# Kernel optimization log

Hardware: AMD Instinct MI355X
Metric: run time of the kernel (lower is better)

Reference implementation:

```python
import jax, jax.numpy as jnp
import numpy as np

NEG_SLOPE = 0.2
EPS = 1e-16

def gatv2(x, edge_index, edge_attr, Wl, bl, We, att, bias):
    """PyG GATv2Conv, heads=1, share_weights=True, with edge_dim."""
    N = x.shape[0]
    h = x @ Wl + bl                      # [N, out] shared lin_l == lin_r
    src, dst = edge_index[0], edge_index[1]
    hj = h[src]                          # source (message) features [E, out]
    hi = h[dst]                          # target features [E, out]
    e = jax.nn.leaky_relu(hi + hj + edge_attr @ We, NEG_SLOPE)  # [E, out]
    score = e @ att                      # [E]
    # segment softmax over edges grouped by destination node
    smax = jax.ops.segment_max(score, dst, num_segments=N)
    ex = jnp.exp(score - smax[dst])
    denom = jax.ops.segment_sum(ex, dst, num_segments=N)
    alpha = ex / (denom[dst] + EPS)      # [E]
    out = jax.ops.segment_sum(hj * alpha[:, None], dst, num_segments=N)
    return out + bias


def setup_inputs() -> dict:
    key = jax.random.key(0)
    N, E = 50000, 800000
    D_IN, D_LAT, D_EDGE, N_ACT = 128, 128, 16, 32
    ks = jax.random.split(key, 16)
    s = 0.05
    inp = {
        "x": jax.random.normal(ks[0], (N, D_IN), jnp.float32),
        "edge_index": jax.random.randint(ks[1], (2, E), 0, N, jnp.int32),
        "edge_attr": jax.random.normal(ks[2], (E, D_EDGE), jnp.float32),
        # gnn_layer: D_IN -> D_LAT
        "Wl1": jax.random.normal(ks[3], (D_IN, D_LAT), jnp.float32) * s,
        "bl1": jnp.zeros((D_LAT,), jnp.float32),
        "We1": jax.random.normal(ks[4], (D_EDGE, D_LAT), jnp.float32) * s,
        "att1": jax.random.normal(ks[5], (D_LAT,), jnp.float32) * s,
        "bias1": jnp.zeros((D_LAT,), jnp.float32),
        # node_layer: D_LAT -> 1
        "Wl2": jax.random.normal(ks[6], (D_LAT, 1), jnp.float32) * s,
        "bl2": jnp.zeros((1,), jnp.float32),
        "We2": jax.random.normal(ks[7], (D_EDGE, 1), jnp.float32) * s,
        "att2": jax.random.normal(ks[8], (1,), jnp.float32) * s,
        "bias2": jnp.zeros((1,), jnp.float32),
        # action_layer: D_LAT -> N_ACT
        "Wl3": jax.random.normal(ks[9], (D_LAT, N_ACT), jnp.float32) * s,
        "bl3": jnp.zeros((N_ACT,), jnp.float32),
        "We3": jax.random.normal(ks[10], (D_EDGE, N_ACT), jnp.float32) * s,
        "att3": jax.random.normal(ks[11], (N_ACT,), jnp.float32) * s,
        "bias3": jnp.zeros((N_ACT,), jnp.float32),
    }
    return inp


def reference(x, edge_index, edge_attr,
              Wl1, bl1, We1, att1, bias1,
              Wl2, bl2, We2, att2, bias2,
              Wl3, bl3, We3, att3, bias3):
    latent = gatv2(x, edge_index, edge_attr, Wl1, bl1, We1, att1, bias1)          # [N, D_LAT]
    node_logits = gatv2(latent, edge_index, edge_attr, Wl2, bl2, We2, att2, bias2)[:, 0]  # [N]
    action_logits = gatv2(latent, edge_index, edge_attr, Wl3, bl3, We3, att3, bias3)      # [N, A]
    # categorical sampling with fixed key (deterministic reference)
    k1, k2 = jax.random.split(jax.random.key(42))
    node_sel = jax.random.categorical(k1, node_logits)
    node_lp = jax.nn.log_softmax(node_logits)[node_sel]
    act_logits_sel = action_logits[node_sel, :]
    action_sel = jax.random.categorical(k2, act_logits_sel)
    action_lp = jax.nn.log_softmax(act_logits_sel)[action_sel]
    return (node_sel, action_sel, node_lp + action_lp)
```

## Files before the change

### kernel.cpp

```cpp
#include <hip/hip_runtime.h>
#include <stdint.h>
#include <math.h>

#define NEG 0.2f
#define TINYF 1.1754943508222875e-38f

typedef float f4 __attribute__((ext_vector_type(4)));
typedef float f2 __attribute__((ext_vector_type(2)));

__host__ __device__ inline void threefry2x32(uint32_t k0, uint32_t k1,
                                             uint32_t x0, uint32_t x1,
                                             uint32_t* o0, uint32_t* o1) {
  uint32_t ks0 = k0, ks1 = k1, ks2 = k0 ^ k1 ^ 0x1BD11BDAu;
  x0 += ks0; x1 += ks1;
#define RR(r) { x0 += x1; x1 = (x1 << (r)) | (x1 >> (32 - (r))); x1 ^= x0; }
  RR(13) RR(15) RR(26) RR(6)
  x0 += ks1; x1 += ks2 + 1u;
  RR(17) RR(29) RR(16) RR(24)
  x0 += ks2; x1 += ks0 + 2u;
  RR(13) RR(15) RR(26) RR(6)
  x0 += ks0; x1 += ks1 + 3u;
  RR(17) RR(29) RR(16) RR(24)
  x0 += ks1; x1 += ks2 + 4u;
  RR(13) RR(15) RR(26) RR(6)
  x0 += ks2; x1 += ks0 + 5u;
#undef RR
  *o0 = x0; *o1 = x1;
}

__device__ inline float gumbel_part(uint32_t ka, uint32_t kb, uint32_t i) {
  uint32_t o0, o1;
  threefry2x32(ka, kb, 0u, i, &o0, &o1);
  uint32_t bits = o0 ^ o1;
  float f = __uint_as_float((bits >> 9) | 0x3f800000u) - 1.0f;
  float u = fmaxf(TINYF, f + TINYF);
  return -logf(-logf(u));
}

__global__ void count_kernel(const int* __restrict__ ei, int E, int* __restrict__ counts) {
  int e = blockIdx.x * blockDim.x + threadIdx.x;
  if (e < E) atomicAdd(&counts[ei[E + e]], 1);
}

#define SCB 256
__global__ __launch_bounds__(256) void scan_partial_kernel(const int* __restrict__ counts,
    int N, int chunk, int* __restrict__ bsum) {
  int b = blockIdx.x;
  int s0 = b * chunk, s1 = s0 + chunk; if (s1 > N) s1 = N;
  int tid = threadIdx.x;
  int v = 0;
  for (int i = s0 + tid; i < s1; i += 256) v += counts[i];
  __shared__ int red[256];
  red[tid] = v; __syncthreads();
  for (int s = 128; s; s >>= 1) { if (tid < s) red[tid] += red[tid + s]; __syncthreads(); }
  if (tid == 0) bsum[b] = red[0];
}

__global__ __launch_bounds__(256) void scan_offsets_kernel(const int* __restrict__ bsum,
    int* __restrict__ boff, int* __restrict__ row_start, int N) {
  int tid = threadIdx.x; int lane = tid & 63; int wv = tid >> 6;
  __shared__ int wsum[4];
  int v = bsum[tid];
  int incl = v;
#pragma unroll
  for (int off = 1; off < 64; off <<= 1) {
    int t = __shfl_up(incl, off);
    if (lane >= off) incl += t;
  }
  if (lane == 63) wsum[wv] = incl;
  __syncthreads();
  if (tid == 0) {
    int s = 0;
    for (int k = 0; k < 4; k++) { int t = wsum[k]; wsum[k] = s; s += t; }
    row_start[N] = s;
  }
  __syncthreads();
  boff[tid] = wsum[wv] + incl - v;
}

__global__ __launch_bounds__(256) void scan_apply_kernel(const int* __restrict__ counts,
    const int* __restrict__ boff, int N, int chunk,
    int* __restrict__ row_start, int* __restrict__ cursor) {
  int b = blockIdx.x;
  int s0 = b * chunk, s1 = s0 + chunk; if (s1 > N) s1 = N;
  int tid = threadIdx.x; int lane = tid & 63; int wv = tid >> 6;
  __shared__ int wsum[4];
  __shared__ int tot_s;
  __shared__ int base_s;
  if (tid == 0) base_s = boff[b];
  __syncthreads();
  for (int c0 = s0; c0 < s1; c0 += 256) {
    int i = c0 + tid;
    int v = (i < s1) ? counts[i] : 0;
    int incl = v;
#pragma unroll
    for (int off = 1; off < 64; off <<= 1) {
      int t = __shfl_up(incl, off);
      if (lane >= off) incl += t;
    }
    if (lane == 63) wsum[wv] = incl;
    __syncthreads();
    if (tid == 0) {
      int s = 0;
      for (int k = 0; k < 4; k++) { int t = wsum[k]; wsum[k] = s; s += t; }
      tot_s = s;
    }
    __syncthreads();
    int base = base_s;
    int excl = base + wsum[wv] + incl - v;
    if (i < s1) { row_start[i] = excl; cursor[i] = excl; }
    __syncthreads();
    if (tid == 0) base_s = base + tot_s;
    __syncthreads();
  }
}

__global__ void scatter_kernel(const int* __restrict__ ei, const float* __restrict__ ea,
                               int E, int* __restrict__ cursor,
                               int* __restrict__ src_csr, float* __restrict__ ea_csr) {
  int e = blockIdx.x * blockDim.x + threadIdx.x;
  if (e < E) {
    int d = ei[E + e];
    int p = atomicAdd(&cursor[d], 1);
    src_csr[p] = ei[e];
    const float4* s4 = (const float4*)&ea[(size_t)e * 16];
    float4* d4 = (float4*)&ea_csr[(size_t)p * 16];
    float4 t0 = s4[0], t1 = s4[1], t2 = s4[2], t3 = s4[3];
    d4[0] = t0; d4[1] = t1; d4[2] = t2; d4[3] = t3;
  }
}

__global__ __launch_bounds__(256) void gemm128_kernel(const float* __restrict__ X,
    const float* __restrict__ W, const float* __restrict__ bias,
    float* __restrict__ out, int M) {
  __shared__ float xs[128][33];
  int row0 = blockIdx.x * 32;
  int tid = threadIdx.x;
  for (int idx = tid; idx < 32 * 128; idx += 256) {
    int r = idx >> 7;
    int k = idx & 127;
    int row = row0 + r;
    xs[k][r] = (row < M) ? X[(size_t)row * 128 + k] : 0.0f;
  }
  __syncthreads();
  int tc = tid & 31, tr = tid >> 5;
  int c0 = tc * 4, r0 = tr * 4;
  float acc[4][4] = {};
#pragma unroll 4
  for (int k = 0; k < 128; k++) {
    float4 w = *(const float4*)&W[k * 128 + c0];
    float x0 = xs[k][r0], x1 = xs[k][r0 + 1], x2 = xs[k][r0 + 2], x3 = xs[k][r0 + 3];
    acc[0][0] += x0 * w.x; acc[0][1] += x0 * w.y; acc[0][2] += x0 * w.z; acc[0][3] += x0 * w.w;
    acc[1][0] += x1 * w.x; acc[1][1] += x1 * w.y; acc[1][2] += x1 * w.z; acc[1][3] += x1 * w.w;
    acc[2][0] += x2 * w.x; acc[2][1] += x2 * w.y; acc[2][2] += x2 * w.z; acc[2][3] += x2 * w.w;
    acc[3][0] += x3 * w.x; acc[3][1] += x3 * w.y; acc[3][2] += x3 * w.z; acc[3][3] += x3 * w.w;
  }
  float4 b4 = *(const float4*)&bias[c0];
  for (int r = 0; r < 4; r++) {
    int row = row0 + r0 + r;
    if (row < M) {
      float4 o;
      o.x = acc[r][0] + b4.x; o.y = acc[r][1] + b4.y;
      o.z = acc[r][2] + b4.z; o.w = acc[r][3] + b4.w;
      *(float4*)&out[(size_t)row * 128 + c0] = o;
    }
  }
}

__global__ __launch_bounds__(256) void gemm32_kernel(const float* __restrict__ X,
    const float* __restrict__ W, const float* __restrict__ bias,
    float* __restrict__ out, int M) {
  int t = blockIdx.x * 256 + threadIdx.x;
  int node = t >> 5, c = t & 31;
  if (node >= M) return;
  const float4* xp = (const float4*)&X[(size_t)node * 128];
  float acc = 0.f;
#pragma unroll
  for (int q = 0; q < 32; q++) {
    float4 x4 = xp[q];
    acc += x4.x * W[(q * 4 + 0) * 32 + c] + x4.y * W[(q * 4 + 1) * 32 + c]
         + x4.z * W[(q * 4 + 2) * 32 + c] + x4.w * W[(q * 4 + 3) * 32 + c];
  }
  out[(size_t)node * 32 + c] = acc + bias[c];
}

__global__ __launch_bounds__(256) void gemv_kernel(const float* __restrict__ X,
    const float* __restrict__ w, const float* __restrict__ b0,
    float* __restrict__ out, int M) {
  int wv = (blockIdx.x * 256 + threadIdx.x) >> 6;
  int lane = threadIdx.x & 63;
  if (wv >= M) return;
  float2 xv = *(const float2*)&X[(size_t)wv * 128 + lane * 2];
  float2 wvv = *(const float2*)&w[lane * 2];
  float v = xv.x * wvv.x + xv.y * wvv.y;
#pragma unroll
  for (int off = 32; off; off >>= 1) v += __shfl_xor(v, off);
  if (lane == 0) out[wv] = v + b0[0];
}

__global__ __launch_bounds__(256) void fused1_kernel(const float* __restrict__ h,
    const int* __restrict__ src_csr, const int* __restrict__ row_start,
    const float* __restrict__ ea_csr,
    const float* __restrict__ We, const float* __restrict__ att,
    const float* __restrict__ bias, float* __restrict__ out, int N) {
  int tid = threadIdx.x;
  int hw = (blockIdx.x * 256 + tid) >> 5;
  int lane = tid & 31;
  if (hw >= N) return;
  int c4 = lane * 4;
  f4 wr0  = *(const f4*)&We[0  * 128 + c4];
  f4 wr1  = *(const f4*)&We[1  * 128 + c4];
  f4 wr2  = *(const f4*)&We[2  * 128 + c4];
  f4 wr3  = *(const f4*)&We[3  * 128 + c4];
  f4 wr4  = *(const f4*)&We[4  * 128 + c4];
  f4 wr5  = *(const f4*)&We[5  * 128 + c4];
  f4 wr6  = *(const f4*)&We[6  * 128 + c4];
  f4 wr7  = *(const f4*)&We[7  * 128 + c4];
  f4 wr8  = *(const f4*)&We[8  * 128 + c4];
  f4 wr9  = *(const f4*)&We[9  * 128 + c4];
  f4 wr10 = *(const f4*)&We[10 * 128 + c4];
  f4 wr11 = *(const f4*)&We[11 * 128 + c4];
  f4 wr12 = *(const f4*)&We[12 * 128 + c4];
  f4 wr13 = *(const f4*)&We[13 * 128 + c4];
  f4 wr14 = *(const f4*)&We[14 * 128 + c4];
  f4 wr15 = *(const f4*)&We[15 * 128 + c4];
  f4 attv = *(const f4*)&att[c4];
  f4 bb = *(const f4*)&bias[c4];
  int start = row_start[hw];
  int deg = row_start[hw + 1] - start;
  if (deg == 0) {
    *(f4*)&out[(size_t)hw * 128 + c4] = bb;
    return;
  }
  f4 hi = *(const f4*)&h[(size_t)hw * 128 + c4];
  int s_l = (lane < deg) ? src_csr[start + lane] : 0;
  int dcap = deg < 32 ? deg : 32;
  const f4* eap = (const f4*)&ea_csr[(size_t)start * 16];
  int dm1 = deg - 1;

  f4 e0 = eap[0], e1 = eap[1], e2 = eap[2], e3 = eap[3];
  int sp0 = __shfl(s_l, 0, 32);
  f4 hj0 = *(const f4*)&h[(size_t)sp0 * 128 + c4];
  int jp1 = (1 < dm1) ? 1 : dm1;
  int sp1 = (jp1 < dcap) ? __shfl(s_l, jp1, 32) : src_csr[start + jp1];
  f4 hj1 = *(const f4*)&h[(size_t)sp1 * 128 + c4];
  int jp2 = (2 < dm1) ? 2 : dm1;
  int sp2 = (jp2 < dcap) ? __shfl(s_l, jp2, 32) : src_csr[start + jp2];
  f4 hj2 = *(const f4*)&h[(size_t)sp2 * 128 + c4];

  float m = -INFINITY, l = 0.f;
  f4 acc = (f4)0.f;
  for (int j = 0; j < deg; j++) {
    f4 hj = hj0; hj0 = hj1; hj1 = hj2;
    f4 ce0 = e0, ce1 = e1, ce2 = e2, ce3 = e3;
    int je = j + 1; if (je > dm1) je = dm1;
    const f4* ep = eap + (size_t)je * 4;
    e0 = ep[0]; e1 = ep[1]; e2 = ep[2]; e3 = ep[3];
    int jn = j + 3; if (jn > dm1) jn = dm1;
    int sn = (jn < dcap) ? __shfl(s_l, jn, 32) : src_csr[start + jn];
    hj2 = *(const f4*)&h[(size_t)sn * 128 + c4];
    f4 v = hi + hj;
    v += ce0.x * wr0  + ce0.y * wr1  + ce0.z * wr2  + ce0.w * wr3;
    v += ce1.x * wr4  + ce1.y * wr5  + ce1.z * wr6  + ce1.w * wr7;
    v += ce2.x * wr8  + ce2.y * wr9  + ce2.z * wr10 + ce2.w * wr11;
    v += ce3.x * wr12 + ce3.y * wr13 + ce3.z * wr14 + ce3.w * wr15;
    v.x = v.x >= 0.f ? v.x : NEG * v.x;
    v.y = v.y >= 0.f ? v.y : NEG * v.y;
    v.z = v.z >= 0.f ? v.z : NEG * v.z;
    v.w = v.w >= 0.f ? v.w : NEG * v.w;
    f4 pv = v * attv;
    float sc = (pv.x + pv.y) + (pv.z + pv.w);
#pragma unroll
    for (int off = 16; off; off >>= 1) sc += __shfl_xor(sc, off);
    float mn = fmaxf(m, sc);
    float scale = __expf(m - mn);
    float w = __expf(sc - mn);
    l = l * scale + w;
    acc = acc * scale + w * hj;
    m = mn;
  }
  float inv = 1.0f / (l + 1e-16f);
  f4 o = acc * inv + bb;
  *(f4*)&out[(size_t)hw * 128 + c4] = o;
}

__global__ __launch_bounds__(256) void fused23_kernel(
    const float* __restrict__ h3, const float* __restrict__ h2,
    const int* __restrict__ src_csr, const int* __restrict__ row_start,
    const float* __restrict__ ea_csr,
    const float* __restrict__ We3, const float* __restrict__ att3,
    const float* __restrict__ bias3, const float* __restrict__ We2,
    const float* __restrict__ att2, const float* __restrict__ bias2,
    float* __restrict__ out3, float* __restrict__ logits, int N) {
  int tid = threadIdx.x;
  int wv = (blockIdx.x * 256 + tid) >> 6;
  int lane = tid & 63;
  if (wv >= N) return;
  int q4 = lane >> 4;
  int l16 = lane & 15;
  int c2 = l16 * 2;
  f2 w3r0  = *(const f2*)&We3[0  * 32 + c2];
  f2 w3r1  = *(const f2*)&We3[1  * 32 + c2];
  f2 w3r2  = *(const f2*)&We3[2  * 32 + c2];
  f2 w3r3  = *(const f2*)&We3[3  * 32 + c2];
  f2 w3r4  = *(const f2*)&We3[4  * 32 + c2];
  f2 w3r5  = *(const f2*)&We3[5  * 32 + c2];
  f2 w3r6  = *(const f2*)&We3[6  * 32 + c2];
  f2 w3r7  = *(const f2*)&We3[7  * 32 + c2];
  f2 w3r8  = *(const f2*)&We3[8  * 32 + c2];
  f2 w3r9  = *(const f2*)&We3[9  * 32 + c2];
  f2 w3r10 = *(const f2*)&We3[10 * 32 + c2];
  f2 w3r11 = *(const f2*)&We3[11 * 32 + c2];
  f2 w3r12 = *(const f2*)&We3[12 * 32 + c2];
  f2 w3r13 = *(const f2*)&We3[13 * 32 + c2];
  f2 w3r14 = *(const f2*)&We3[14 * 32 + c2];
  f2 w3r15 = *(const f2*)&We3[15 * 32 + c2];
  float u0 = We2[0],  u1 = We2[1],  u2 = We2[2],  u3 = We2[3];
  float u4 = We2[4],  u5 = We2[5],  u6 = We2[6],  u7 = We2[7];
  float u8 = We2[8],  u9 = We2[9],  u10 = We2[10], u11 = We2[11];
  float u12 = We2[12], u13 = We2[13], u14 = We2[14], u15 = We2[15];
  f2 at3 = *(const f2*)&att3[c2];
  float a2s = att2[0];
  f2 bi3 = *(const f2*)&bias3[c2];
  int start = row_start[wv];
  int deg = row_start[wv + 1] - start;
  if (deg == 0) {
    if (lane < 16) *(f2*)&out3[(size_t)wv * 32 + c2] = bi3;
    if (lane == 0) logits[wv] = bias2[0];
    return;
  }
  f2 hi3 = *(const f2*)&h3[(size_t)wv * 32 + c2];
  float hi2 = h2[wv];
  int s_l = (lane < deg) ? src_csr[start + lane] : 0;
  int dcap = deg < 64 ? deg : 64;
  const float4* eap = (const float4*)&ea_csr[(size_t)start * 16];
  float m3 = -INFINITY, l3 = 0.f; f2 a3 = (f2)0.f;
  float m2 = -INFINITY, l2 = 0.f; float a2 = 0.f;
  for (int j = q4; j < deg; j += 4) {
    int s = (j < dcap) ? __shfl(s_l, j) : src_csr[start + j];
    f2 hj3 = *(const f2*)&h3[(size_t)s * 32 + c2];
    float h2s = h2[s];
    float4 c0 = eap[(size_t)j * 4 + 0];
    float4 c1 = eap[(size_t)j * 4 + 1];
    float4 cc2 = eap[(size_t)j * 4 + 2];
    float4 c3 = eap[(size_t)j * 4 + 3];
    f2 v = hi3 + hj3;
    v += c0.x * w3r0;   v += c0.y * w3r1;
    v += c0.z * w3r2;   v += c0.w * w3r3;
    v += c1.x * w3r4;   v += c1.y * w3r5;
    v += c1.z * w3r6;   v += c1.w * w3r7;
    v += cc2.x * w3r8;  v += cc2.y * w3r9;
    v += cc2.z * w3r10; v += cc2.w * w3r11;
    v += c3.x * w3r12;  v += c3.y * w3r13;
    v += c3.z * w3r14;  v += c3.w * w3r15;
    v.x = v.x >= 0.f ? v.x : NEG * v.x;
    v.y = v.y >= 0.f ? v.y : NEG * v.y;
    float t3 = v.x * at3.x + v.y * at3.y;
#pragma unroll
    for (int off = 8; off; off >>= 1) t3 += __shfl_xor(t3, off);
    float v2 = hi2 + h2s;
    v2 += c0.x * u0   + c0.y * u1   + c0.z * u2   + c0.w * u3;
    v2 += c1.x * u4   + c1.y * u5   + c1.z * u6   + c1.w * u7;
    v2 += cc2.x * u8  + cc2.y * u9  + cc2.z * u10 + cc2.w * u11;
    v2 += c3.x * u12  + c3.y * u13  + c3.z * u14  + c3.w * u15;
    v2 = v2 >= 0.f ? v2 : NEG * v2;
    float t2 = v2 * a2s;
    float mn3 = fmaxf(m3, t3);
    float sc3 = __expf(m3 - mn3);
    float w3 = __expf(t3 - mn3);
    l3 = l3 * sc3 + w3;
    a3 = a3 * sc3 + w3 * hj3;
    m3 = mn3;
    float mn2 = fmaxf(m2, t2);
    float sc2 = __expf(m2 - mn2);
    float w2 = __expf(t2 - mn2);
    l2 = l2 * sc2 + w2;
    a2 = a2 * sc2 + w2 * h2s;
    m2 = mn2;
  }
#pragma unroll
  for (int off = 16; off <= 32; off <<= 1) {
    float m3o = __shfl_xor(m3, off), l3o = __shfl_xor(l3, off);
    float ax = __shfl_xor(a3.x, off), ay = __shfl_xor(a3.y, off);
    float M3 = fmaxf(m3, m3o);
    float sA = (m3 == -INFINITY) ? 0.f : __expf(m3 - M3);
    float sB = (m3o == -INFINITY) ? 0.f : __expf(m3o - M3);
    l3 = l3 * sA + l3o * sB;
    a3.x = a3.x * sA + ax * sB;
    a3.y = a3.y * sA + ay * sB;
    m3 = M3;
    float m2o = __shfl_xor(m2, off), l2o = __shfl_xor(l2, off);
    float az = __shfl_xor(a2, off);
    float M2 = fmaxf(m2, m2o);
    float tA = (m2 == -INFINITY) ? 0.f : __expf(m2 - M2);
    float tB = (m2o == -INFINITY) ? 0.f : __expf(m2o - M2);
    l2 = l2 * tA + l2o * tB;
    a2 = a2 * tA + az * tB;
    m2 = M2;
  }
  if (lane < 16) {
    f2 o;
    o.x = a3.x / (l3 + 1e-16f) + bi3.x;
    o.y = a3.y / (l3 + 1e-16f) + bi3.y;
    *(f2*)&out3[(size_t)wv * 32 + c2] = o;
  }
  if (lane == 0) logits[wv] = a2 / (l2 + 1e-16f) + bias2[0];
}

#define NSB 64
__global__ __launch_bounds__(256) void node_partial_kernel(const float* __restrict__ logits,
    int N, uint32_t ka, uint32_t kb,
    float* __restrict__ pB, int* __restrict__ pI,
    float* __restrict__ pM, float* __restrict__ pL) {
  int chunk = (N + NSB - 1) / NSB;
  int s0 = blockIdx.x * chunk;
  int s1 = s0 + chunk; if (s1 > N) s1 = N;
  int tid = threadIdx.x;
  float best = -INFINITY; int bi = 0x7fffffff;
  float m = -INFINITY, l = 0.f;
  for (int i = s0 + tid; i < s1; i += 256) {
    float lg = logits[i];
    float mn = fmaxf(m, lg);
    l = l * __expf(m - mn) + __expf(lg - mn);
    m = mn;
    float v = lg + gumbel_part(ka, kb, (uint32_t)i);
    if (v > best) { best = v; bi = i; }
  }
  __shared__ float sb[256], sm[256], sl[256];
  __shared__ int si[256];
  sb[tid] = best; si[tid] = bi; sm[tid] = m; sl[tid] = l;
  __syncthreads();
  for (int s = 128; s; s >>= 1) {
    if (tid < s) {
      if (sb[tid + s] > sb[tid] || (sb[tid + s] == sb[tid] && si[tid + s] < si[tid])) {
        sb[tid] = sb[tid + s]; si[tid] = si[tid + s];
      }
      float M = fmaxf(sm[tid], sm[tid + s]);
      float t0 = (sm[tid] == -INFINITY) ? 0.f : sl[tid] * __expf(sm[tid] - M);
      float t1 = (sm[tid + s] == -INFINITY) ? 0.f : sl[tid + s] * __expf(sm[tid + s] - M);
      sm[tid] = M; sl[tid] = t0 + t1;
    }
    __syncthreads();
  }
  if (tid == 0) { pB[blockIdx.x] = sb[0]; pI[blockIdx.x] = si[0]; pM[blockIdx.x] = sm[0]; pL[blockIdx.x] = sl[0]; }
}

__global__ __launch_bounds__(64) void node_final_kernel(const float* __restrict__ logits,
    const float* __restrict__ pB, const int* __restrict__ pI,
    const float* __restrict__ pM, const float* __restrict__ pL,
    float* __restrict__ scal) {
  int lane = threadIdx.x;
  float best = pB[lane]; int bi = pI[lane];
  float m = pM[lane]; float l = pL[lane];
#pragma unroll
  for (int off = 32; off; off >>= 1) {
    float ob = __shfl_xor(best, off); int oi = __shfl_xor(bi, off);
    if (ob > best || (ob == best && oi < bi)) { best = ob; bi = oi; }
    float om = __shfl_xor(m, off); float ol = __shfl_xor(l, off);
    float M = fmaxf(m, om);
    float t0 = (m == -INFINITY) ? 0.f : l * __expf(m - M);
    float t1 = (om == -INFINITY) ? 0.f : ol * __expf(om - M);
    m = M; l = t0 + t1;
  }
  if (lane == 0) {
    ((int*)scal)[0] = bi;
    scal[3] = logits[bi] - (m + logf(l));
  }
}

__global__ __launch_bounds__(64) void action_kernel(const float* __restrict__ out3,
    const float* __restrict__ scal, uint32_t ka, uint32_t kb,
    float* __restrict__ dout, int out_size) {
  int lane = threadIdx.x;
  int sel = ((const int*)scal)[0];
  float v = -INFINITY, noisy = -INFINITY;
  if (lane < 32) {
    v = out3[(size_t)sel * 32 + lane];
    noisy = v + gumbel_part(ka, kb, (uint32_t)lane);
  }
  int idx = lane;
  float nv = noisy;
#pragma unroll
  for (int off = 32; off; off >>= 1) {
    float ov = __shfl_xor(nv, off);
    int oi = __shfl_xor(idx, off);
    if (ov > nv || (ov == nv && oi < idx)) { nv = ov; idx = oi; }
  }
  float vm = v;
#pragma unroll
  for (int off = 32; off; off >>= 1) vm = fmaxf(vm, __shfl_xor(vm, off));
  float ex = (lane < 32) ? expf(v - vm) : 0.f;
#pragma unroll
  for (int off = 32; off; off >>= 1) ex += __shfl_xor(ex, off);
  float vsel = __shfl(v, idx);
  if (lane == 0) {
    float action_lp = vsel - vm - logf(ex);
    dout[0] = (float)sel;
    dout[1] = (float)idx;
    dout[2] = scal[3] + action_lp;
  }
  for (int i = 3 + lane; i < out_size; i += 64) dout[i] = 0.f;
}

extern "C" void kernel_launch(void* const* d_in, const int* in_sizes, int n_in,
                              void* d_out, int out_size, void* d_ws, size_t ws_size,
                              hipStream_t stream) {
  const float* x     = (const float*)d_in[0];
  const int*   ei    = (const int*)d_in[1];
  const float* ea    = (const float*)d_in[2];
  const float* Wl1   = (const float*)d_in[3];
  const float* bl1   = (const float*)d_in[4];
  const float* We1   = (const float*)d_in[5];
  const float* att1  = (const float*)d_in[6];
  const float* bias1 = (const float*)d_in[7];
  const float* Wl2   = (const float*)d_in[8];
  const float* bl2   = (const float*)d_in[9];
  const float* We2   = (const float*)d_in[10];
  const float* att2  = (const float*)d_in[11];
  const float* bias2 = (const float*)d_in[12];
  const float* Wl3   = (const float*)d_in[13];
  const float* bl3   = (const float*)d_in[14];
  const float* We3   = (const float*)d_in[15];
  const float* att3  = (const float*)d_in[16];
  const float* bias3 = (const float*)d_in[17];
  int N = in_sizes[0] / 128;
  int E = in_sizes[1] / 2;
  float* out = (float*)d_out;

  char* p = (char*)d_ws;
  auto alloc = [&](size_t bytes) -> char* {
    char* r = p; p += (bytes + 255) & ~(size_t)255; return r;
  };
  float* h1      = (float*)alloc((size_t)N * 128 * 4);
  float* latent  = (float*)alloc((size_t)N * 128 * 4);
  float* h3      = (float*)alloc((size_t)N * 32 * 4);
  float* h2      = (float*)alloc((size_t)N * 4);
  float* logits  = (float*)alloc((size_t)N * 4);
  float* out3    = (float*)alloc((size_t)N * 32 * 4);
  int* counts    = (int*)alloc((size_t)N * 4);
  int* row_start = (int*)alloc((size_t)(N + 1) * 4);
  int* cursor    = (int*)alloc((size_t)N * 4);
  int* src_csr   = (int*)alloc((size_t)E * 4);
  float* ea_csr  = (float*)alloc((size_t)E * 16 * 4);
  int* bsum      = (int*)alloc(SCB * 4);
  int* boff      = (int*)alloc(SCB * 4);
  float* pB      = (float*)alloc(NSB * 4);
  int*   pI      = (int*)alloc(NSB * 4);
  float* pM      = (float*)alloc(NSB * 4);
  float* pL      = (float*)alloc(NSB * 4);
  float* scal    = (float*)alloc(64);
  (void)ws_size; (void)n_in;

  uint32_t k1a, k1b, k2a, k2b;
  threefry2x32(0u, 42u, 0u, 0u, &k1a, &k1b);
  threefry2x32(0u, 42u, 0u, 1u, &k2a, &k2b);

  int chunk = (N + SCB - 1) / SCB;

  hipMemsetAsync(counts, 0, (size_t)N * 4, stream);
  count_kernel<<<(E + 255) / 256, 256, 0, stream>>>(ei, E, counts);
  scan_partial_kernel<<<SCB, 256, 0, stream>>>(counts, N, chunk, bsum);
  scan_offsets_kernel<<<1, 256, 0, stream>>>(bsum, boff, row_start, N);
  scan_apply_kernel<<<SCB, 256, 0, stream>>>(counts, boff, N, chunk, row_start, cursor);
  scatter_kernel<<<(E + 255) / 256, 256, 0, stream>>>(ei, ea, E, cursor, src_csr, ea_csr);

  gemm128_kernel<<<(N + 31) / 32, 256, 0, stream>>>(x, Wl1, bl1, h1, N);
  fused1_kernel<<<(N + 7) / 8, 256, 0, stream>>>(h1, src_csr, row_start,
                                                 ea_csr, We1, att1, bias1, latent, N);

  gemm32_kernel<<<((size_t)N * 32 + 255) / 256, 256, 0, stream>>>(latent, Wl3, bl3, h3, N);
  gemv_kernel<<<(N + 3) / 4, 256, 0, stream>>>(latent, Wl2, bl2, h2, N);

  fused23_kernel<<<(N + 3) / 4, 256, 0, stream>>>(h3, h2, src_csr, row_start, ea_csr,
                                                  We3, att3, bias3, We2, att2, bias2,
                                                  out3, logits, N);

  node_partial_kernel<<<NSB, 256, 0, stream>>>(logits, N, k1a, k1b, pB, pI, pM, pL);
  node_final_kernel<<<1, 64, 0, stream>>>(logits, pB, pI, pM, pL, scal);
  action_kernel<<<1, 64, 0, stream>>>(out3, scal, k2a, k2b, out, out_size);
}
```

Baseline: 591.9 us.

## Split GAT layers into edge-parallel scoring and node-parallel aggregation

Each fused per-destination GAT kernel becomes two kernels. An edge-parallel kernel computes attention weights exp(min(score,60)) into a per-edge buffer using a new dst_csr array. A node-parallel kernel then gathers source features and does a plain weighted sum, with no online-softmax rescaling. This aims to balance load across skewed degrees and shorten the serial dependency chain, at the cost of extra global traffic for the weight buffer and dst indices. Dropping the max subtraction and clamping scores at 60 changes numerics and could overflow or lose precision for large scores.

```diff
diff --git a/kernel.cpp b/kernel.cpp
--- a/kernel.cpp
+++ b/kernel.cpp
@@ -117,12 +117,14 @@
 
 __global__ void scatter_kernel(const int* __restrict__ ei, const float* __restrict__ ea,
                                int E, int* __restrict__ cursor,
-                               int* __restrict__ src_csr, float* __restrict__ ea_csr) {
+                               int* __restrict__ src_csr, int* __restrict__ dst_csr,
+                               float* __restrict__ ea_csr) {
   int e = blockIdx.x * blockDim.x + threadIdx.x;
   if (e < E) {
     int d = ei[E + e];
     int p = atomicAdd(&cursor[d], 1);
     src_csr[p] = ei[e];
+    dst_csr[p] = d;
     const float4* s4 = (const float4*)&ea[(size_t)e * 16];
     float4* d4 = (float4*)&ea_csr[(size_t)p * 16];
     float4 t0 = s4[0], t1 = s4[1], t2 = s4[2], t3 = s4[3];
@@ -198,15 +200,19 @@
   if (lane == 0) out[wv] = v + b0[0];
 }
 
-__global__ __launch_bounds__(256) void fused1_kernel(const float* __restrict__ h,
-    const int* __restrict__ src_csr, const int* __restrict__ row_start,
+#define EPH 8
+__global__ __launch_bounds__(256, 3) void edge_score1_kernel(
+    const float* __restrict__ h,
+    const int* __restrict__ src_csr, const int* __restrict__ dst_csr,
     const float* __restrict__ ea_csr,
     const float* __restrict__ We, const float* __restrict__ att,
-    const float* __restrict__ bias, float* __restrict__ out, int N) {
+    float* __restrict__ w_csr, int E) {
   int tid = threadIdx.x;
+  int lane = tid & 31;
   int hw = (blockIdx.x * 256 + tid) >> 5;
-  int lane = tid & 31;
-  if (hw >= N) return;
+  int e0 = hw * EPH;
+  if (e0 >= E) return;
+  int e1 = e0 + EPH; if (e1 > E) e1 = E;
   int c4 = lane * 4;
   f4 wr0  = *(const f4*)&We[0  * 128 + c4];
   f4 wr1  = *(const f4*)&We[1  * 128 + c4];
@@ -225,6 +231,65 @@
   f4 wr14 = *(const f4*)&We[14 * 128 + c4];
   f4 wr15 = *(const f4*)&We[15 * 128 + c4];
   f4 attv = *(const f4*)&att[c4];
+  for (int e = e0; e < e1; e += 2) {
+    int eB = e + 1;
+    int hasB = (eB < e1);
+    int eBc = hasB ? eB : e;
+    int sA = src_csr[e];   int dA = dst_csr[e];
+    int sB = src_csr[eBc]; int dB = dst_csr[eBc];
+    f4 hjA = *(const f4*)&h[(size_t)sA * 128 + c4];
+    f4 hiA = *(const f4*)&h[(size_t)dA * 128 + c4];
+    f4 hjB = *(const f4*)&h[(size_t)sB * 128 + c4];
+    f4 hiB = *(const f4*)&h[(size_t)dB * 128 + c4];
+    const f4* eAp = (const f4*)&ea_csr[(size_t)e * 16];
+    const f4* eBp = (const f4*)&ea_csr[(size_t)eBc * 16];
+    f4 a0 = eAp[0], a1 = eAp[1], a2 = eAp[2], a3 = eAp[3];
+    f4 b0 = eBp[0], b1 = eBp[1], b2 = eBp[2], b3 = eBp[3];
+    f4 vA = hiA + hjA;
+    f4 vB = hiB + hjB;
+    vA += a0.x * wr0  + a0.y * wr1  + a0.z * wr2  + a0.w * wr3;
+    vB += b0.x * wr0  + b0.y * wr1  + b0.z * wr2  + b0.w * wr3;
+    vA += a1.x * wr4  + a1.y * wr5  + a1.z * wr6  + a1.w * wr7;
+    vB += b1.x * wr4  + b1.y * wr5  + b1.z * wr6  + b1.w * wr7;
+    vA += a2.x * wr8  + a2.y * wr9  + a2.z * wr10 + a2.w * wr11;
+    vB += b2.x * wr8  + b2.y * wr9  + b2.z * wr10 + b2.w * wr11;
+    vA += a3.x * wr12 + a3.y * wr13 + a3.z * wr14 + a3.w * wr15;
+    vB += b3.x * wr12 + b3.y * wr13 + b3.z * wr14 + b3.w * wr15;
+    vA.x = vA.x >= 0.f ? vA.x : NEG * vA.x;
+    vA.y = vA.y >= 0.f ? vA.y : NEG * vA.y;
+    vA.z = vA.z >= 0.f ? vA.z : NEG * vA.z;
+    vA.w = vA.w >= 0.f ? vA.w : NEG * vA.w;
+    vB.x = vB.x >= 0.f ? vB.x : NEG * vB.x;
+    vB.y = vB.y >= 0.f ? vB.y : NEG * vB.y;
+    vB.z = vB.z >= 0.f ? vB.z : NEG * vB.z;
+    vB.w = vB.w >= 0.f ? vB.w : NEG * vB.w;
+    f4 pA = vA * attv;
+    f4 pB = vB * attv;
+    float scA = (pA.x + pA.y) + (pA.z + pA.w);
+    float scB = (pB.x + pB.y) + (pB.z + pB.w);
+#pragma unroll
+    for (int off = 16; off; off >>= 1) {
+      scA += __shfl_xor(scA, off);
+      scB += __shfl_xor(scB, off);
+    }
+    float wA = __expf(fminf(scA, 60.f));
+    float wB = __expf(fminf(scB, 60.f));
+    if (lane == 0) {
+      w_csr[e] = wA;
+      if (hasB) w_csr[eB] = wB;
+    }
+  }
+}
+
+__global__ __launch_bounds__(256) void aggregate1_kernel(
+    const float* __restrict__ h, const int* __restrict__ src_csr,
+    const int* __restrict__ row_start, const float* __restrict__ w_csr,
+    const float* __restrict__ bias, float* __restrict__ out, int N) {
+  int tid = threadIdx.x;
+  int hw = (blockIdx.x * 256 + tid) >> 5;
+  int lane = tid & 31;
+  if (hw >= N) return;
+  int c4 = lane * 4;
   f4 bb = *(const f4*)&bias[c4];
   int start = row_start[hw];
   int deg = row_start[hw + 1] - start;
@@ -232,72 +297,56 @@
     *(f4*)&out[(size_t)hw * 128 + c4] = bb;
     return;
   }
-  f4 hi = *(const f4*)&h[(size_t)hw * 128 + c4];
   int s_l = (lane < deg) ? src_csr[start + lane] : 0;
   int dcap = deg < 32 ? deg : 32;
-  const f4* eap = (const f4*)&ea_csr[(size_t)start * 16];
   int dm1 = deg - 1;
-
-  f4 e0 = eap[0], e1 = eap[1], e2 = eap[2], e3 = eap[3];
-  int sp0 = __shfl(s_l, 0, 32);
-  f4 hj0 = *(const f4*)&h[(size_t)sp0 * 128 + c4];
-  int jp1 = (1 < dm1) ? 1 : dm1;
-  int sp1 = (jp1 < dcap) ? __shfl(s_l, jp1, 32) : src_csr[start + jp1];
-  f4 hj1 = *(const f4*)&h[(size_t)sp1 * 128 + c4];
-  int jp2 = (2 < dm1) ? 2 : dm1;
-  int sp2 = (jp2 < dcap) ? __shfl(s_l, jp2, 32) : src_csr[start + jp2];
-  f4 hj2 = *(const f4*)&h[(size_t)sp2 * 128 + c4];
-
-  float m = -INFINITY, l = 0.f;
+  int jc1 = dm1 < 1 ? dm1 : 1;
+  int jc2 = dm1 < 2 ? dm1 : 2;
+  int jc3 = dm1 < 3 ? dm1 : 3;
+  int s0 = __shfl(s_l, 0, 32);
+  int s1 = (jc1 < dcap) ? __shfl(s_l, jc1, 32) : src_csr[start + jc1];
+  int s2 = (jc2 < dcap) ? __shfl(s_l, jc2, 32) : src_csr[start + jc2];
+  int s3 = (jc3 < dcap) ? __shfl(s_l, jc3, 32) : src_csr[start + jc3];
+  f4 p0 = *(const f4*)&h[(size_t)s0 * 128 + c4];
+  float w0v = w_csr[start + 0];
+  f4 p1 = *(const f4*)&h[(size_t)s1 * 128 + c4];
+  float w1v = w_csr[start + jc1];
+  f4 p2 = *(const f4*)&h[(size_t)s2 * 128 + c4];
+  float w2v = w_csr[start + jc2];
+  f4 p3 = *(const f4*)&h[(size_t)s3 * 128 + c4];
+  float w3v = w_csr[start + jc3];
   f4 acc = (f4)0.f;
+  float l = 0.f;
   for (int j = 0; j < deg; j++) {
-    f4 hj = hj0; hj0 = hj1; hj1 = hj2;
-    f4 ce0 = e0, ce1 = e1, ce2 = e2, ce3 = e3;
-    int je = j + 1; if (je > dm1) je = dm1;
-    const f4* ep = eap + (size_t)je * 4;
-    e0 = ep[0]; e1 = ep[1]; e2 = ep[2]; e3 = ep[3];
-    int jn = j + 3; if (jn > dm1) jn = dm1;
+    f4 cur = p0; float cw = w0v;
+    p0 = p1; w0v = w1v;
+    p1 = p2; w1v = w2v;
+    p2 = p3; w2v = w3v;
+    int jn = j + 4; if (jn > dm1) jn = dm1;
     int sn = (jn < dcap) ? __shfl(s_l, jn, 32) : src_csr[start + jn];
-    hj2 = *(const f4*)&h[(size_t)sn * 128 + c4];
-    f4 v = hi + hj;
-    v += ce0.x * wr0  + ce0.y * wr1  + ce0.z * wr2  + ce0.w * wr3;
-    v += ce1.x * wr4  + ce1.y * wr5  + ce1.z * wr6  + ce1.w * wr7;
-    v += ce2.x * wr8  + ce2.y * wr9  + ce2.z * wr10 + ce2.w * wr11;
-    v += ce3.x * wr12 + ce3.y * wr13 + ce3.z * wr14 + ce3.w * wr15;
-    v.x = v.x >= 0.f ? v.x : NEG * v.x;
-    v.y = v.y >= 0.f ? v.y : NEG * v.y;
-    v.z = v.z >= 0.f ? v.z : NEG * v.z;
-    v.w = v.w >= 0.f ? v.w : NEG * v.w;
-    f4 pv = v * attv;
-    float sc = (pv.x + pv.y) + (pv.z + pv.w);
-#pragma unroll
-    for (int off = 16; off; off >>= 1) sc += __shfl_xor(sc, off);
-    float mn = fmaxf(m, sc);
-    float scale = __expf(m - mn);
-    float w = __expf(sc - mn);
-    l = l * scale + w;
-    acc = acc * scale + w * hj;
-    m = mn;
+    w3v = w_csr[start + jn];
+    p3 = *(const f4*)&h[(size_t)sn * 128 + c4];
+    acc += cw * cur;
+    l += cw;
   }
   float inv = 1.0f / (l + 1e-16f);
-  f4 o = acc * inv + bb;
-  *(f4*)&out[(size_t)hw * 128 + c4] = o;
-}
-
-__global__ __launch_bounds__(256) void fused23_kernel(
+  *(f4*)&out[(size_t)hw * 128 + c4] = acc * inv + bb;
+}
+
+#define EPQ 8
+__global__ __launch_bounds__(256, 3) void edge_score23_kernel(
     const float* __restrict__ h3, const float* __restrict__ h2,
-    const int* __restrict__ src_csr, const int* __restrict__ row_start,
+    const int* __restrict__ src_csr, const int* __restrict__ dst_csr,
     const float* __restrict__ ea_csr,
     const float* __restrict__ We3, const float* __restrict__ att3,
-    const float* __restrict__ bias3, const float* __restrict__ We2,
-    const float* __restrict__ att2, const float* __restrict__ bias2,
-    float* __restrict__ out3, float* __restrict__ logits, int N) {
+    const float* __restrict__ We2v, const float* __restrict__ att2,
+    float* __restrict__ w23, int E) {
   int tid = threadIdx.x;
-  int wv = (blockIdx.x * 256 + tid) >> 6;
-  int lane = tid & 63;
-  if (wv >= N) return;
-  int q4 = lane >> 4;
-  int l16 = lane & 15;
+  int l16 = tid & 15;
+  int qw = (blockIdx.x * 256 + tid) >> 4;
+  int e0 = qw * EPQ;
+  if (e0 >= E) return;
+  int e1 = e0 + EPQ; if (e1 > E) e1 = E;
   int c2 = l16 * 2;
   f2 w3r0  = *(const f2*)&We3[0  * 32 + c2];
   f2 w3r1  = *(const f2*)&We3[1  * 32 + c2];
@@ -315,96 +364,107 @@
   f2 w3r13 = *(const f2*)&We3[13 * 32 + c2];
   f2 w3r14 = *(const f2*)&We3[14 * 32 + c2];
   f2 w3r15 = *(const f2*)&We3[15 * 32 + c2];
-  float u0 = We2[0],  u1 = We2[1],  u2 = We2[2],  u3 = We2[3];
-  float u4 = We2[4],  u5 = We2[5],  u6 = We2[6],  u7 = We2[7];
-  float u8 = We2[8],  u9 = We2[9],  u10 = We2[10], u11 = We2[11];
-  float u12 = We2[12], u13 = We2[13], u14 = We2[14], u15 = We2[15];
+  float u = We2v[l16];
   f2 at3 = *(const f2*)&att3[c2];
   float a2s = att2[0];
-  f2 bi3 = *(const f2*)&bias3[c2];
-  int start = row_start[wv];
-  int deg = row_start[wv + 1] - start;
-  if (deg == 0) {
-    if (lane < 16) *(f2*)&out3[(size_t)wv * 32 + c2] = bi3;
-    if (lane == 0) logits[wv] = bias2[0];
-    return;
-  }
-  f2 hi3 = *(const f2*)&h3[(size_t)wv * 32 + c2];
-  float hi2 = h2[wv];
-  int s_l = (lane < deg) ? src_csr[start + lane] : 0;
-  int dcap = deg < 64 ? deg : 64;
-  const float4* eap = (const float4*)&ea_csr[(size_t)start * 16];
-  float m3 = -INFINITY, l3 = 0.f; f2 a3 = (f2)0.f;
-  float m2 = -INFINITY, l2 = 0.f; float a2 = 0.f;
-  for (int j = q4; j < deg; j += 4) {
-    int s = (j < dcap) ? __shfl(s_l, j) : src_csr[start + j];
-    f2 hj3 = *(const f2*)&h3[(size_t)s * 32 + c2];
+  for (int e = e0; e < e1; e++) {
+    int s = src_csr[e];
+    int d = dst_csr[e];
+    f2 hj = *(const f2*)&h3[(size_t)s * 32 + c2];
+    f2 hi = *(const f2*)&h3[(size_t)d * 32 + c2];
     float h2s = h2[s];
-    float4 c0 = eap[(size_t)j * 4 + 0];
-    float4 c1 = eap[(size_t)j * 4 + 1];
-    float4 cc2 = eap[(size_t)j * 4 + 2];
-    float4 c3 = eap[(size_t)j * 4 + 3];
-    f2 v = hi3 + hj3;
-    v += c0.x * w3r0;   v += c0.y * w3r1;
-    v += c0.z * w3r2;   v += c0.w * w3r3;
-    v += c1.x * w3r4;   v += c1.y * w3r5;
-    v += c1.z * w3r6;   v += c1.w * w3r7;
-    v += cc2.x * w3r8;  v += cc2.y * w3r9;
-    v += cc2.z * w3r10; v += cc2.w * w3r11;
-    v += c3.x * w3r12;  v += c3.y * w3r13;
-    v += c3.z * w3r14;  v += c3.w * w3r15;
+    float h2i = h2[d];
+    const float4* ep = (const float4*)&ea_csr[(size_t)e * 16];
+    float4 c0 = ep[0], c1 = ep[1], cq = ep[2], c3 = ep[3];
+    float eav = ea_csr[(size_t)e * 16 + l16];
+    f2 v = hi + hj;
+    v += c0.x * w3r0;  v += c0.y * w3r1;
+    v += c0.z * w3r2;  v += c0.w * w3r3;
+    v += c1.x * w3r4;  v += c1.y * w3r5;
+    v += c1.z * w3r6;  v += c1.w * w3r7;
+    v += cq.x * w3r8;  v += cq.y * w3r9;
+    v += cq.z * w3r10; v += cq.w * w3r11;
+    v += c3.x * w3r12; v += c3.y * w3r13;
+    v += c3.z * w3r14; v += c3.w * w3r15;
     v.x = v.x >= 0.f ? v.x : NEG * v.x;
     v.y = v.y >= 0.f ? v.y : NEG * v.y;
     float t3 = v.x * at3.x + v.y * at3.y;
-#pragma unroll
-    for (int off = 8; off; off >>= 1) t3 += __shfl_xor(t3, off);
-    float v2 = hi2 + h2s;
-    v2 += c0.x * u0   + c0.y * u1   + c0.z * u2   + c0.w * u3;
-    v2 += c1.x * u4   + c1.y * u5   + c1.z * u6   + c1.w * u7;
-    v2 += cc2.x * u8  + cc2.y * u9  + cc2.z * u10 + cc2.w * u11;
-    v2 += c3.x * u12  + c3.y * u13  + c3.z * u14  + c3.w * u15;
+    float p2 = eav * u;
+#pragma unroll
+    for (int off = 8; off; off >>= 1) {
+      t3 += __shfl_xor(t3, off);
+      p2 += __shfl_xor(p2, off);
+    }
+    float v2 = h2i + h2s + p2;
     v2 = v2 >= 0.f ? v2 : NEG * v2;
     float t2 = v2 * a2s;
-    float mn3 = fmaxf(m3, t3);
-    float sc3 = __expf(m3 - mn3);
-    float w3 = __expf(t3 - mn3);
-    l3 = l3 * sc3 + w3;
-    a3 = a3 * sc3 + w3 * hj3;
-    m3 = mn3;
-    float mn2 = fmaxf(m2, t2);
-    float sc2 = __expf(m2 - mn2);
-    float w2 = __expf(t2 - mn2);
-    l2 = l2 * sc2 + w2;
-    a2 = a2 * sc2 + w2 * h2s;
-    m2 = mn2;
-  }
-#pragma unroll
-  for (int off = 16; off <= 32; off <<= 1) {
-    float m3o = __shfl_xor(m3, off), l3o = __shfl_xor(l3, off);
-    float ax = __shfl_xor(a3.x, off), ay = __shfl_xor(a3.y, off);
-    float M3 = fmaxf(m3, m3o);
-    float sA = (m3 == -INFINITY) ? 0.f : __expf(m3 - M3);
-    float sB = (m3o == -INFINITY) ? 0.f : __expf(m3o - M3);
-    l3 = l3 * sA + l3o * sB;
-    a3.x = a3.x * sA + ax * sB;
-    a3.y = a3.y * sA + ay * sB;
-    m3 = M3;
-    float m2o = __shfl_xor(m2, off), l2o = __shfl_xor(l2, off);
-    float az = __shfl_xor(a2, off);
-    float M2 = fmaxf(m2, m2o);
-    float tA = (m2 == -INFINITY) ? 0.f : __expf(m2 - M2);
-    float tB = (m2o == -INFINITY) ? 0.f : __expf(m2o - M2);
-    l2 = l2 * tA + l2o * tB;
-    a2 = a2 * tA + az * tB;
-    m2 = M2;
-  }
-  if (lane < 16) {
-    f2 o;
-    o.x = a3.x / (l3 + 1e-16f) + bi3.x;
-    o.y = a3.y / (l3 + 1e-16f) + bi3.y;
-    *(f2*)&out3[(size_t)wv * 32 + c2] = o;
-  }
-  if (lane == 0) logits[wv] = a2 / (l2 + 1e-16f) + bias2[0];
+    float w3e = __expf(fminf(t3, 60.f));
+    float w2e = __expf(fminf(t2, 60.f));
+    if (l16 == 0) {
+      f2 wp; wp.x = w3e; wp.y = w2e;
+      *(f2*)&w23[(size_t)2 * e] = wp;
+    }
+  }
+}
+
+__global__ __launch_bounds__(256) void aggregate23_kernel(
+    const float* __restrict__ h3, const float* __restrict__ h2,
+    const int* __restrict__ src_csr, const int* __restrict__ row_start,
+    const float* __restrict__ w23,
+    const float* __restrict__ bias3, const float* __restrict__ bias2,
+    float* __restrict__ out3, float* __restrict__ logits, int N) {
+  int tid = threadIdx.x;
+  int hw = (blockIdx.x * 256 + tid) >> 5;
+  int lane = tid & 31;
+  if (hw >= N) return;
+  float b3v = bias3[lane];
+  int start = row_start[hw];
+  int deg = row_start[hw + 1] - start;
+  if (deg == 0) {
+    out3[(size_t)hw * 32 + lane] = b3v;
+    if (lane == 0) logits[hw] = bias2[0];
+    return;
+  }
+  int s_l = (lane < deg) ? src_csr[start + lane] : 0;
+  int dcap = deg < 32 ? deg : 32;
+  int dm1 = deg - 1;
+  int jc1 = dm1 < 1 ? dm1 : 1;
+  int jc2 = dm1 < 2 ? dm1 : 2;
+  int jc3 = dm1 < 3 ? dm1 : 3;
+  int s0 = __shfl(s_l, 0, 32);
+  int s1 = (jc1 < dcap) ? __shfl(s_l, jc1, 32) : src_csr[start + jc1];
+  int s2 = (jc2 < dcap) ? __shfl(s_l, jc2, 32) : src_csr[start + jc2];
+  int s3 = (jc3 < dcap) ? __shfl(s_l, jc3, 32) : src_csr[start + jc3];
+  float p0 = h3[(size_t)s0 * 32 + lane];
+  float q0 = h2[s0];
+  f2 w0v = *(const f2*)&w23[(size_t)2 * (start + 0)];
+  float p1 = h3[(size_t)s1 * 32 + lane];
+  float q1 = h2[s1];
+  f2 w1v = *(const f2*)&w23[(size_t)2 * (start + jc1)];
+  float p2 = h3[(size_t)s2 * 32 + lane];
+  float q2 = h2[s2];
+  f2 w2v = *(const f2*)&w23[(size_t)2 * (start + jc2)];
+  float p3 = h3[(size_t)s3 * 32 + lane];
+  float q3 = h2[s3];
+  f2 w3v = *(const f2*)&w23[(size_t)2 * (start + jc3)];
+  float acc3 = 0.f, l3 = 0.f, acc2 = 0.f, l2 = 0.f;
+  for (int j = 0; j < deg; j++) {
+    float cur3 = p0; float cur2 = q0; f2 cw = w0v;
+    p0 = p1; q0 = q1; w0v = w1v;
+    p1 = p2; q1 = q2; w1v = w2v;
+    p2 = p3; q2 = q3; w2v = w3v;
+    int jn = j + 4; if (jn > dm1) jn = dm1;
+    int sn = (jn < dcap) ? __shfl(s_l, jn, 32) : src_csr[start + jn];
+    w3v = *(const f2*)&w23[(size_t)2 * (start + jn)];
+    p3 = h3[(size_t)sn * 32 + lane];
+    q3 = h2[sn];
+    acc3 += cw.x * cur3;
+    l3 += cw.x;
+    acc2 += cw.y * cur2;
+    l2 += cw.y;
+  }
+  out3[(size_t)hw * 32 + lane] = acc3 / (l3 + 1e-16f) + b3v;
+  if (lane == 0) logits[hw] = acc2 / (l2 + 1e-16f) + bias2[0];
 }
 
 #define NSB 64
@@ -541,7 +601,10 @@
   int* row_start = (int*)alloc((size_t)(N + 1) * 4);
   int* cursor    = (int*)alloc((size_t)N * 4);
   int* src_csr   = (int*)alloc((size_t)E * 4);
+  int* dst_csr   = (int*)alloc((size_t)E * 4);
   float* ea_csr  = (float*)alloc((size_t)E * 16 * 4);
+  float* w1_csr  = (float*)alloc((size_t)E * 4);
+  float* w23_csr = (float*)alloc((size_t)E * 8);
   int* bsum      = (int*)alloc(SCB * 4);
   int* boff      = (int*)alloc(SCB * 4);
   float* pB      = (float*)alloc(NSB * 4);
@@ -562,18 +625,24 @@
   scan_partial_kernel<<<SCB, 256, 0, stream>>>(counts, N, chunk, bsum);
   scan_offsets_kernel<<<1, 256, 0, stream>>>(bsum, boff, row_start, N);
   scan_apply_kernel<<<SCB, 256, 0, stream>>>(counts, boff, N, chunk, row_start, cursor);
-  scatter_kernel<<<(E + 255) / 256, 256, 0, stream>>>(ei, ea, E, cursor, src_csr, ea_csr);
+  scatter_kernel<<<(E + 255) / 256, 256, 0, stream>>>(ei, ea, E, cursor, src_csr, dst_csr, ea_csr);
 
   gemm128_kernel<<<(N + 31) / 32, 256, 0, stream>>>(x, Wl1, bl1, h1, N);
-  fused1_kernel<<<(N + 7) / 8, 256, 0, stream>>>(h1, src_csr, row_start,
-                                                 ea_csr, We1, att1, bias1, latent, N);
+
+  int hws1 = (E + EPH - 1) / EPH;
+  edge_score1_kernel<<<(hws1 + 7) / 8, 256, 0, stream>>>(h1, src_csr, dst_csr, ea_csr,
+                                                         We1, att1, w1_csr, E);
+  aggregate1_kernel<<<(N + 7) / 8, 256, 0, stream>>>(h1, src_csr, row_start, w1_csr,
+                                                     bias1, latent, N);
 
   gemm32_kernel<<<((size_t)N * 32 + 255) / 256, 256, 0, stream>>>(latent, Wl3, bl3, h3, N);
   gemv_kernel<<<(N + 3) / 4, 256, 0, stream>>>(latent, Wl2, bl2, h2, N);
 
-  fused23_kernel<<<(N + 3) / 4, 256, 0, stream>>>(h3, h2, src_csr, row_start, ea_csr,
-                                                  We3, att3, bias3, We2, att2, bias2,
-                                                  out3, logits, N);
+  int qws = (E + EPQ - 1) / EPQ;
+  edge_score23_kernel<<<(qws + 15) / 16, 256, 0, stream>>>(h3, h2, src_csr, dst_csr, ea_csr,
+                                                           We3, att3, We2, att2, w23_csr, E);
+  aggregate23_kernel<<<(N + 7) / 8, 256, 0, stream>>>(h3, h2, src_csr, row_start, w23_csr,
+                                                      bias3, bias2, out3, logits, N);
 
   node_partial_kernel<<<NSB, 256, 0, stream>>>(logits, N, k1a, k1b, pB, pI, pM, pL);
   node_final_kernel<<<1, 64, 0, stream>>>(logits, pB, pI, pM, pL, scal);
```

New measurement: 720.2 us. 21.7% more time.
